# Kernel tuning notes

Measured on AMD Instinct MI355X. Metric: run time of the kernel, lower is better.

## Reference

```python
import jax, jax.numpy as jnp
import numpy as np

LATENT, COND, NEURONS, NHID = 64, 96, 128, 3
EPS = 1e-5


def setup_inputs() -> dict:
    key = jax.random.key(0)
    ks = jax.random.split(key, 20)
    B, N = 1024, 512
    z0 = jax.random.normal(ks[0], (B, LATENT), jnp.float32)
    # monotone time grid in [0,1]
    t = jnp.cumsum(jax.random.uniform(ks[1], (B, N, 1), jnp.float32), axis=1)
    t = t / t[:, -1:, :]
    condition = jax.random.normal(ks[2], (B, N, COND), jnp.float32)
    dims = [LATENT + COND] + [NEURONS] * NHID
    inp = {"z0": z0, "t": t, "condition": condition}
    for i in range(NHID):
        din, dout = dims[i], dims[i + 1]
        inp[f"W{i}"] = jax.random.normal(ks[3 + 4 * i], (din, dout), jnp.float32) / np.sqrt(din)
        inp[f"b{i}"] = jnp.zeros((dout,), jnp.float32)
        inp[f"g{i}"] = jnp.ones((dout,), jnp.float32)
        inp[f"beta{i}"] = jnp.zeros((dout,), jnp.float32)
    inp["Wo"] = jax.random.normal(ks[16], (NEURONS, LATENT), jnp.float32) / np.sqrt(NEURONS)
    inp["bo"] = jnp.zeros((LATENT,), jnp.float32)
    return inp


def _layer_norm(x, g, b):
    mu = jnp.mean(x, axis=-1, keepdims=True)
    var = jnp.var(x, axis=-1, keepdims=True)
    return (x - mu) * jax.lax.rsqrt(var + EPS) * g + b


def reference(z0, t, condition,
              W0, b0, g0, beta0,
              W1, b1, g1, beta1,
              W2, b2, g2, beta2,
              Wo, bo):
    # dropout is inference-mode identity
    hidden = [(W0, b0, g0, beta0), (W1, b1, g1, beta1), (W2, b2, g2, beta2)]

    def mlp(x):
        h = x
        for (W, b, g, be) in hidden:
            h = jnp.tanh(_layer_norm(h @ W + b, g, be))
        return h @ Wo + bo

    # time-major sequences for scan: [N-1, B, ...]
    cond_seq = jnp.swapaxes(condition[:, :-1, :], 0, 1)
    dt_seq = jnp.swapaxes(t[:, 1:, 0] - t[:, :-1, 0], 0, 1)[..., None]

    def step(z, inp):
        cond_i, dt_i = inp
        dz = mlp(jnp.concatenate([z, cond_i], axis=-1))
        z_next = z + dt_i * dz
        return z_next, z_next

    _, zs = jax.lax.scan(step, z0, (cond_seq, dt_seq))  # [N-1, B, D]
    z_traj = jnp.concatenate([z0[None], zs], axis=0)  # [N, B, D]
    return jnp.swapaxes(z_traj, 0, 1)  # [B, N, D]
```

## Files before the change

kernel.cpp:

```cpp
#include <hip/hip_runtime.h>
#include <stdint.h>

#define NSEQ 512
#define XS 168
#define AS 136
#define PS 36
#define EPS 1e-5f

typedef short bfrag __attribute__((ext_vector_type(8)));
typedef float f4 __attribute__((ext_vector_type(4)));
#define MFMA16 __builtin_amdgcn_mfma_f32_16x16x32_bf16

__device__ __forceinline__ unsigned short f2bf(float f){
  uint32_t u = __float_as_uint(f);
  u += 0x7FFFu + ((u>>16)&1u);
  return (unsigned short)(u>>16);
}
__device__ __forceinline__ uint32_t pk2bf(float a, float b){
  uint32_t r;
  asm("v_cvt_pk_bf16_f32 %0, %1, %2" : "=v"(r) : "v"(a), "v"(b));
  return r;
}
__device__ __forceinline__ float tanh_fast(float v){
  float e = __builtin_amdgcn_exp2f(v * 2.8853900817779268f);
  float r = __builtin_amdgcn_rcpf(e + 1.f);
  return fmaf(-2.f, r, 1.f);
}
__device__ __forceinline__ void lds_barrier(){
  asm volatile("s_waitcnt lgkmcnt(0)" ::: "memory");
  __builtin_amdgcn_s_barrier();
  asm volatile("" ::: "memory");
}

__device__ __forceinline__ void stats_write(const float (&h0)[4], const float (&h1)[4],
                                            float* __restrict__ part,
                                            const int w, const int lg, const int lc){
  const float s = ((h0[0]+h0[1])+(h0[2]+h0[3])) + ((h1[0]+h1[1])+(h1[2]+h1[3]));
  const float q = (fmaf(h0[0],h0[0], h0[1]*h0[1]) + fmaf(h0[2],h0[2], h0[3]*h0[3]))
                + (fmaf(h1[0],h1[0], h1[1]*h1[1]) + fmaf(h1[2],h1[2], h1[3]*h1[3]));
  *(float2*)(part + lc*PS + (w*4+lg)*2) = make_float2(s, q);
}

__device__ __forceinline__ void ln_tanh_store(const float (&h0)[4], const float (&h1)[4],
    const float (&gd)[2][4], const float (&bed)[2][4],
    const float* __restrict__ part, unsigned short* __restrict__ actb,
    const int w, const int lg, const int lc){
  const float* pr = part + lc*PS;
  const f4 p0=*(const f4*)(pr),    p1=*(const f4*)(pr+4),  p2=*(const f4*)(pr+8),  p3=*(const f4*)(pr+12);
  const f4 p4=*(const f4*)(pr+16), p5=*(const f4*)(pr+20), p6=*(const f4*)(pr+24), p7=*(const f4*)(pr+28);
  const float ss = (((p0.x+p0.z)+(p1.x+p1.z)) + ((p2.x+p2.z)+(p3.x+p3.z)))
                 + (((p4.x+p4.z)+(p5.x+p5.z)) + ((p6.x+p6.z)+(p7.x+p7.z)));
  const float qq = (((p0.y+p0.w)+(p1.y+p1.w)) + ((p2.y+p2.w)+(p3.y+p3.w)))
                 + (((p4.y+p4.w)+(p5.y+p5.w)) + ((p6.y+p6.w)+(p7.y+p7.w)));
  const float mu = ss * 0.0078125f;
  const float rs = rsqrtf(fmaf(qq, 0.0078125f, -mu*mu) + EPS);
  float e0[4], e1[4];
#pragma unroll
  for (int g=0; g<4; ++g){
    e0[g] = tanh_fast(fmaf((h0[g]-mu)*rs, gd[0][g], bed[0][g]));
    e1[g] = tanh_fast(fmaf((h1[g]-mu)*rs, gd[1][g], bed[1][g]));
  }
  uint4 pk4;
  pk4.x = pk2bf(e0[0],e0[1]); pk4.y = pk2bf(e0[2],e0[3]);
  pk4.z = pk2bf(e1[0],e1[1]); pk4.w = pk2bf(e1[2],e1[3]);
  *(uint4*)(actb + lc*AS + w*32 + lg*8) = pk4;
}

__global__ __launch_bounds__(256, 1)
void latent_ode_v9(const float* __restrict__ z0, const float* __restrict__ tt,
                   const float* __restrict__ cond,
                   const float* __restrict__ W0, const float* __restrict__ b0,
                   const float* __restrict__ g0, const float* __restrict__ be0,
                   const float* __restrict__ W1, const float* __restrict__ b1,
                   const float* __restrict__ g1, const float* __restrict__ be1,
                   const float* __restrict__ W2, const float* __restrict__ b2,
                   const float* __restrict__ g2, const float* __restrict__ be2,
                   const float* __restrict__ Wo, const float* __restrict__ bo,
                   float* __restrict__ out)
{
  __shared__ __align__(16) unsigned short xin[16*XS];
  __shared__ __align__(16) unsigned short act[16*AS];
  __shared__ __align__(16) float part[16*PS];

  const int t  = threadIdx.x;
  const int w  = t >> 6;
  const int l  = t & 63;
  const int lg = l >> 4;
  const int lc = l & 15;
  const int r0 = blockIdx.x * 16;
  const int zcol = w*16 + lg*4;

  bfrag A0z[2][2], A0c[2][3], A1f[2][4], A2f[2][4], Aof[4];
#pragma unroll
  for (int nt=0; nt<2; ++nt){
    const int col = w*32 + nt*4 + ((lc>>2)<<3) + (lc&3);
#pragma unroll
    for (int kt=0; kt<2; ++kt){
      union { bfrag v; unsigned short u[8]; } r;
#pragma unroll
      for (int j=0; j<8; ++j) r.u[j] = f2bf(W0[(size_t)(kt*32 + lg*8 + j)*128 + col]);
      A0z[nt][kt] = r.v;
    }
#pragma unroll
    for (int s=0; s<3; ++s){
      union { bfrag v; unsigned short u[8]; } r;
#pragma unroll
      for (int j=0; j<8; ++j) r.u[j] = f2bf(W0[(size_t)(64 + s*32 + lg*8 + j)*128 + col]);
      A0c[nt][s] = r.v;
    }
#pragma unroll
    for (int kt=0; kt<4; ++kt){
      union { bfrag v; unsigned short u[8]; } r1, r2;
#pragma unroll
      for (int j=0; j<8; ++j){
        const int k = kt*32 + lg*8 + j;
        r1.u[j] = f2bf(W1[(size_t)k*128 + col]);
        r2.u[j] = f2bf(W2[(size_t)k*128 + col]);
      }
      A1f[nt][kt] = r1.v; A2f[nt][kt] = r2.v;
    }
  }
#pragma unroll
  for (int kt=0; kt<4; ++kt){
    union { bfrag v; unsigned short u[8]; } r;
#pragma unroll
    for (int j=0; j<8; ++j)
      r.u[j] = f2bf(Wo[(size_t)(kt*32 + lg*8 + j)*64 + (w*16 + lc)]);
    Aof[kt] = r.v;
  }
  float bd0[2][4], gd0[2][4], bed0[2][4];
  float bd1[2][4], gd1[2][4], bed1[2][4];
  float bd2[2][4], gd2[2][4], bed2[2][4];
  float bo_d[4];
#pragma unroll
  for (int nt=0; nt<2; ++nt){
#pragma unroll
    for (int g=0; g<4; ++g){
      const int n = w*32 + lg*8 + nt*4 + g;
      bd0[nt][g]=b0[n]; gd0[nt][g]=g0[n]; bed0[nt][g]=be0[n];
      bd1[nt][g]=b1[n]; gd1[nt][g]=g1[n]; bed1[nt][g]=be1[n];
      bd2[nt][g]=b2[n]; gd2[nt][g]=g2[n]; bed2[nt][g]=be2[n];
    }
  }
#pragma unroll
  for (int g=0; g<4; ++g) bo_d[g] = bo[zcol + g];

  const float* tp = tt + (size_t)(r0+lc)*NSEQ;
  float tcv = tp[0], tnv = tp[1];

  f4 zr;
  {
    const f4 zv = *(const f4*)(z0 + (size_t)(r0+lc)*64 + zcol);
    zr = zv;
    *(f4*)(out + ((size_t)(r0+lc)*NSEQ)*64 + zcol) = zv;
    *(uint2*)(xin + lc*XS + zcol) = make_uint2(pk2bf(zv[0],zv[1]), pk2bf(zv[2],zv[3]));
  }

  const bool stgW = (t < 192);
  const int srow = t / 12, s8 = t - srow*12;
  const float* cptr = cond + ((size_t)(r0+srow)*NSEQ)*96 + s8*8;
  float4 pf0 = {0,0,0,0}, pf1 = {0,0,0,0};
  if (stgW){
    const float4 c0 = *(const float4*)(cptr);
    const float4 c1 = *(const float4*)(cptr + 4);
    uint4 u;
    u.x = pk2bf(c0.x,c0.y); u.y = pk2bf(c0.z,c0.w);
    u.z = pk2bf(c1.x,c1.y); u.w = pk2bf(c1.z,c1.w);
    *(uint4*)(xin + srow*XS + 64 + s8*8) = u;
    pf0 = *(const float4*)(cptr + 96);
    pf1 = *(const float4*)(cptr + 100);
  }
  lds_barrier();

  f4 apC[2];
  {
    const int o = lc*XS + 64 + lg*8;
    const bfrag c0 = *(const bfrag*)(xin + o);
    const bfrag c1 = *(const bfrag*)(xin + o + 32);
    const bfrag c2 = *(const bfrag*)(xin + o + 64);
    const f4 z4 = {0,0,0,0};
#pragma unroll
    for (int nt=0; nt<2; ++nt){
      f4 a = MFMA16(A0c[nt][0], c0, z4, 0,0,0);
      a = MFMA16(A0c[nt][1], c1, a, 0,0,0);
      a = MFMA16(A0c[nt][2], c2, a, 0,0,0);
      apC[nt] = a;
    }
  }
  lds_barrier();

  float h0[4], h1[4];
  for (int i=0; i<NSEQ-1; ++i){
    const int ip2 = (i+2 <= NSEQ-1) ? (i+2) : (NSEQ-1);
    const float tfv = tp[ip2];
    {
      const int o = lc*XS + lg*8;
      const bfrag bz0 = *(const bfrag*)(xin + o);
      const bfrag bz1 = *(const bfrag*)(xin + o + 32);
      const f4 z4 = {0,0,0,0};
      f4 c0 = MFMA16(A0z[0][0], bz0, z4, 0,0,0);
      f4 c1 = MFMA16(A0z[1][0], bz0, z4, 0,0,0);
      c0 = MFMA16(A0z[0][1], bz1, c0, 0,0,0);
      c1 = MFMA16(A0z[1][1], bz1, c1, 0,0,0);
#pragma unroll
      for (int g=0; g<4; ++g){
        h0[g] = (c0[g] + apC[0][g]) + bd0[0][g];
        h1[g] = (c1[g] + apC[1][g]) + bd0[1][g];
      }
      stats_write(h0, h1, part, w, lg, lc);
    }
    if (stgW){
      uint4 u;
      u.x = pk2bf(pf0.x,pf0.y); u.y = pk2bf(pf0.z,pf0.w);
      u.z = pk2bf(pf1.x,pf1.y); u.w = pk2bf(pf1.z,pf1.w);
      *(uint4*)(xin + srow*XS + 64 + s8*8) = u;
      if (i < NSEQ-2){
        pf0 = *(const float4*)(cptr + (size_t)(i+2)*96);
        pf1 = *(const float4*)(cptr + (size_t)(i+2)*96 + 4);
      }
    }
    lds_barrier();

    {
      const int o = lc*XS + 64 + lg*8;
      const bfrag c0 = *(const bfrag*)(xin + o);
      const bfrag c1 = *(const bfrag*)(xin + o + 32);
      const bfrag c2 = *(const bfrag*)(xin + o + 64);
      const f4 z4 = {0,0,0,0};
      f4 a0 = MFMA16(A0c[0][0], c0, z4, 0,0,0);
      f4 a1 = MFMA16(A0c[1][0], c0, z4, 0,0,0);
      a0 = MFMA16(A0c[0][1], c1, a0, 0,0,0);
      a1 = MFMA16(A0c[1][1], c1, a1, 0,0,0);
      a0 = MFMA16(A0c[0][2], c2, a0, 0,0,0);
      a1 = MFMA16(A0c[1][2], c2, a1, 0,0,0);
      ln_tanh_store(h0, h1, gd0, bed0, part, act, w, lg, lc);
      apC[0] = a0; apC[1] = a1;
    }
    lds_barrier();

    {
      const int o = lc*AS + lg*8;
      const bfrag b0f = *(const bfrag*)(act + o);
      const bfrag b1f = *(const bfrag*)(act + o + 32);
      const bfrag b2f = *(const bfrag*)(act + o + 64);
      const bfrag b3f = *(const bfrag*)(act + o + 96);
      const f4 z4 = {0,0,0,0};
      f4 ca0 = MFMA16(A1f[0][0], b0f, z4, 0,0,0);
      f4 cb0 = MFMA16(A1f[0][1], b1f, z4, 0,0,0);
      f4 ca1 = MFMA16(A1f[1][0], b0f, z4, 0,0,0);
      f4 cb1 = MFMA16(A1f[1][1], b1f, z4, 0,0,0);
      ca0 = MFMA16(A1f[0][2], b2f, ca0, 0,0,0);
      cb0 = MFMA16(A1f[0][3], b3f, cb0, 0,0,0);
      ca1 = MFMA16(A1f[1][2], b2f, ca1, 0,0,0);
      cb1 = MFMA16(A1f[1][3], b3f, cb1, 0,0,0);
#pragma unroll
      for (int g=0; g<4; ++g){
        h0[g] = (ca0[g]+cb0[g]) + bd1[0][g];
        h1[g] = (ca1[g]+cb1[g]) + bd1[1][g];
      }
      stats_write(h0, h1, part, w, lg, lc);
    }
    lds_barrier();

    ln_tanh_store(h0, h1, gd1, bed1, part, act, w, lg, lc);
    lds_barrier();

    {
      const int o = lc*AS + lg*8;
      const bfrag b0f = *(const bfrag*)(act + o);
      const bfrag b1f = *(const bfrag*)(act + o + 32);
      const bfrag b2f = *(const bfrag*)(act + o + 64);
      const bfrag b3f = *(const bfrag*)(act + o + 96);
      const f4 z4 = {0,0,0,0};
      f4 ca0 = MFMA16(A2f[0][0], b0f, z4, 0,0,0);
      f4 cb0 = MFMA16(A2f[0][1], b1f, z4, 0,0,0);
      f4 ca1 = MFMA16(A2f[1][0], b0f, z4, 0,0,0);
      f4 cb1 = MFMA16(A2f[1][1], b1f, z4, 0,0,0);
      ca0 = MFMA16(A2f[0][2], b2f, ca0, 0,0,0);
      cb0 = MFMA16(A2f[0][3], b3f, cb0, 0,0,0);
      ca1 = MFMA16(A2f[1][2], b2f, ca1, 0,0,0);
      cb1 = MFMA16(A2f[1][3], b3f, cb1, 0,0,0);
#pragma unroll
      for (int g=0; g<4; ++g){
        h0[g] = (ca0[g]+cb0[g]) + bd2[0][g];
        h1[g] = (ca1[g]+cb1[g]) + bd2[1][g];
      }
      stats_write(h0, h1, part, w, lg, lc);
    }
    lds_barrier();

    ln_tanh_store(h0, h1, gd2, bed2, part, act, w, lg, lc);
    lds_barrier();

    {
      const int o = lc*AS + lg*8;
      const bfrag b0f = *(const bfrag*)(act + o);
      const bfrag b1f = *(const bfrag*)(act + o + 32);
      const bfrag b2f = *(const bfrag*)(act + o + 64);
      const bfrag b3f = *(const bfrag*)(act + o + 96);
      const f4 z4 = {0,0,0,0};
      f4 aa = MFMA16(Aof[0], b0f, z4, 0,0,0);
      f4 ab = MFMA16(Aof[1], b1f, z4, 0,0,0);
      aa = MFMA16(Aof[2], b2f, aa, 0,0,0);
      ab = MFMA16(Aof[3], b3f, ab, 0,0,0);
      const float dt = tnv - tcv;
      f4 zn;
#pragma unroll
      for (int g=0; g<4; ++g) zn[g] = fmaf(dt, (aa[g]+ab[g]) + bo_d[g], zr[g]);
      zr = zn;
      *(f4*)(out + ((size_t)(r0+lc)*NSEQ + (size_t)(i+1))*64 + zcol) = zn;
      *(uint2*)(xin + lc*XS + zcol) = make_uint2(pk2bf(zn[0],zn[1]), pk2bf(zn[2],zn[3]));
      tcv = tnv; tnv = tfv;
    }
    lds_barrier();
  }
}

extern "C" void kernel_launch(void* const* d_in, const int* in_sizes, int n_in,
                              void* d_out, int out_size, void* d_ws, size_t ws_size,
                              hipStream_t stream) {
  const float* z0   = (const float*)d_in[0];
  const float* tt   = (const float*)d_in[1];
  const float* cond = (const float*)d_in[2];
  const float* W0   = (const float*)d_in[3];
  const float* b0   = (const float*)d_in[4];
  const float* g0   = (const float*)d_in[5];
  const float* be0  = (const float*)d_in[6];
  const float* W1   = (const float*)d_in[7];
  const float* b1   = (const float*)d_in[8];
  const float* g1   = (const float*)d_in[9];
  const float* be1  = (const float*)d_in[10];
  const float* W2   = (const float*)d_in[11];
  const float* b2   = (const float*)d_in[12];
  const float* g2   = (const float*)d_in[13];
  const float* be2  = (const float*)d_in[14];
  const float* Wo   = (const float*)d_in[15];
  const float* bo   = (const float*)d_in[16];
  float* out = (float*)d_out;

  hipLaunchKernelGGL(latent_ode_v9, dim3(64), dim3(256), 0, stream,
                     z0, tt, cond, W0, b0, g0, be0, W1, b1, g1, be1,
                     W2, b2, g2, be2, Wo, bo, out);
}
```

Before: 1.111 ms.

## Fuse LayerNorm+tanh into consumer GEMM to halve per-step barriers

```diff
diff --git a/kernel.cpp b/kernel.cpp
--- a/kernel.cpp
+++ b/kernel.cpp
@@ -2,9 +2,10 @@
 #include <stdint.h>
 
 #define NSEQ 512
-#define XS 168
-#define AS 136
+#define XS 104
+#define HS 132
 #define PS 36
+#define ZS 76
 #define EPS 1e-5f
 
 typedef short bfrag __attribute__((ext_vector_type(8)));
@@ -41,10 +42,8 @@
   *(float2*)(part + lc*PS + (w*4+lg)*2) = make_float2(s, q);
 }
 
-__device__ __forceinline__ void ln_tanh_store(const float (&h0)[4], const float (&h1)[4],
-    const float (&gd)[2][4], const float (&bed)[2][4],
-    const float* __restrict__ part, unsigned short* __restrict__ actb,
-    const int w, const int lg, const int lc){
+__device__ __forceinline__ void ln_mu_rs(const float* __restrict__ part, const int lc,
+                                         float& mu, float& rs){
   const float* pr = part + lc*PS;
   const f4 p0=*(const f4*)(pr),    p1=*(const f4*)(pr+4),  p2=*(const f4*)(pr+8),  p3=*(const f4*)(pr+12);
   const f4 p4=*(const f4*)(pr+16), p5=*(const f4*)(pr+20), p6=*(const f4*)(pr+24), p7=*(const f4*)(pr+28);
@@ -52,35 +51,55 @@
                  + (((p4.x+p4.z)+(p5.x+p5.z)) + ((p6.x+p6.z)+(p7.x+p7.z)));
   const float qq = (((p0.y+p0.w)+(p1.y+p1.w)) + ((p2.y+p2.w)+(p3.y+p3.w)))
                  + (((p4.y+p4.w)+(p5.y+p5.w)) + ((p6.y+p6.w)+(p7.y+p7.w)));
-  const float mu = ss * 0.0078125f;
-  const float rs = rsqrtf(fmaf(qq, 0.0078125f, -mu*mu) + EPS);
-  float e0[4], e1[4];
-#pragma unroll
-  for (int g=0; g<4; ++g){
-    e0[g] = tanh_fast(fmaf((h0[g]-mu)*rs, gd[0][g], bed[0][g]));
-    e1[g] = tanh_fast(fmaf((h1[g]-mu)*rs, gd[1][g], bed[1][g]));
-  }
-  uint4 pk4;
-  pk4.x = pk2bf(e0[0],e0[1]); pk4.y = pk2bf(e0[2],e0[3]);
-  pk4.z = pk2bf(e1[0],e1[1]); pk4.w = pk2bf(e1[2],e1[3]);
-  *(uint4*)(actb + lc*AS + w*32 + lg*8) = pk4;
+  mu = ss * 0.0078125f;
+  rs = rsqrtf(fmaf(qq, 0.0078125f, -mu*mu) + EPS);
+}
+
+__device__ __forceinline__ void consume_ln(const float* __restrict__ hb,
+    const float* __restrict__ part, const uint32_t* __restrict__ pg,
+    bfrag (&B)[4], const int lg, const int lc){
+  float mu, rs;
+  ln_mu_rs(part, lc, mu, rs);
+#pragma unroll
+  for (int kt=0; kt<4; ++kt){
+    const float* hp = hb + lc*HS + kt*32 + lg*8;
+    const f4 ha = *(const f4*)(hp);
+    const f4 hc = *(const f4*)(hp + 4);
+    const uint4 q0 = *(const uint4*)(pg + kt*32 + lg*8);
+    const uint4 q1 = *(const uint4*)(pg + kt*32 + lg*8 + 4);
+    const uint32_t gu[8] = {q0.x,q0.y,q0.z,q0.w,q1.x,q1.y,q1.z,q1.w};
+    float e[8];
+#pragma unroll
+    for (int j=0;j<8;++j){
+      const float h = (j<4)? ha[j] : hc[j-4];
+      const float gg = __uint_as_float(gu[j] & 0xFFFF0000u);
+      const float bb = __uint_as_float(gu[j] << 16);
+      e[j] = tanh_fast(fmaf((h - mu)*rs, gg, bb));
+    }
+    union { bfrag v; uint32_t u[4]; } r;
+    r.u[0]=pk2bf(e[0],e[1]); r.u[1]=pk2bf(e[2],e[3]);
+    r.u[2]=pk2bf(e[4],e[5]); r.u[3]=pk2bf(e[6],e[7]);
+    B[kt]=r.v;
+  }
 }
 
 __global__ __launch_bounds__(256, 1)
-void latent_ode_v9(const float* __restrict__ z0, const float* __restrict__ tt,
-                   const float* __restrict__ cond,
-                   const float* __restrict__ W0, const float* __restrict__ b0,
-                   const float* __restrict__ g0, const float* __restrict__ be0,
-                   const float* __restrict__ W1, const float* __restrict__ b1,
-                   const float* __restrict__ g1, const float* __restrict__ be1,
-                   const float* __restrict__ W2, const float* __restrict__ b2,
-                   const float* __restrict__ g2, const float* __restrict__ be2,
-                   const float* __restrict__ Wo, const float* __restrict__ bo,
-                   float* __restrict__ out)
+void latent_ode_v15(const float* __restrict__ z0, const float* __restrict__ tt,
+                    const float* __restrict__ cond,
+                    const float* __restrict__ W0, const float* __restrict__ b0,
+                    const float* __restrict__ g0, const float* __restrict__ be0,
+                    const float* __restrict__ W1, const float* __restrict__ b1,
+                    const float* __restrict__ g1, const float* __restrict__ be1,
+                    const float* __restrict__ W2, const float* __restrict__ b2,
+                    const float* __restrict__ g2, const float* __restrict__ be2,
+                    const float* __restrict__ Wo, const float* __restrict__ bo,
+                    float* __restrict__ out)
 {
   __shared__ __align__(16) unsigned short xin[16*XS];
-  __shared__ __align__(16) unsigned short act[16*AS];
-  __shared__ __align__(16) float part[16*PS];
+  __shared__ __align__(16) unsigned short zbuf[16*ZS];
+  __shared__ __align__(16) float hA[16*HS], hB[16*HS];
+  __shared__ __align__(16) float partA[16*PS], partB[16*PS];
+  __shared__ __align__(16) uint32_t pgb[3*128];
 
   const int t  = threadIdx.x;
   const int w  = t >> 6;
@@ -128,22 +147,26 @@
       r.u[j] = f2bf(Wo[(size_t)(kt*32 + lg*8 + j)*64 + (w*16 + lc)]);
     Aof[kt] = r.v;
   }
-  float bd0[2][4], gd0[2][4], bed0[2][4];
-  float bd1[2][4], gd1[2][4], bed1[2][4];
-  float bd2[2][4], gd2[2][4], bed2[2][4];
-  float bo_d[4];
+  float bd0[2][4], bd1[2][4], bd2[2][4], bo_d[4];
 #pragma unroll
   for (int nt=0; nt<2; ++nt){
 #pragma unroll
     for (int g=0; g<4; ++g){
       const int n = w*32 + lg*8 + nt*4 + g;
-      bd0[nt][g]=b0[n]; gd0[nt][g]=g0[n]; bed0[nt][g]=be0[n];
-      bd1[nt][g]=b1[n]; gd1[nt][g]=g1[n]; bed1[nt][g]=be1[n];
-      bd2[nt][g]=b2[n]; gd2[nt][g]=g2[n]; bed2[nt][g]=be2[n];
+      bd0[nt][g]=b0[n]; bd1[nt][g]=b1[n]; bd2[nt][g]=b2[n];
     }
   }
 #pragma unroll
   for (int g=0; g<4; ++g) bo_d[g] = bo[zcol + g];
+
+  for (int idx=t; idx<384; idx+=256){
+    const int n = idx & 127;
+    float gv, bv;
+    if (idx < 128){ gv = g0[n]; bv = be0[n]; }
+    else if (idx < 256){ gv = g1[n]; bv = be1[n]; }
+    else { gv = g2[n]; bv = be2[n]; }
+    pgb[idx] = pk2bf(bv, gv);
+  }
 
   const float* tp = tt + (size_t)(r0+lc)*NSEQ;
   float tcv = tp[0], tnv = tp[1];
@@ -152,8 +175,8 @@
   {
     const f4 zv = *(const f4*)(z0 + (size_t)(r0+lc)*64 + zcol);
     zr = zv;
+    *(uint2*)(zbuf + lc*ZS + zcol) = make_uint2(pk2bf(zv[0],zv[1]), pk2bf(zv[2],zv[3]));
     *(f4*)(out + ((size_t)(r0+lc)*NSEQ)*64 + zcol) = zv;
-    *(uint2*)(xin + lc*XS + zcol) = make_uint2(pk2bf(zv[0],zv[1]), pk2bf(zv[2],zv[3]));
   }
 
   const bool stgW = (t < 192);
@@ -166,7 +189,7 @@
     uint4 u;
     u.x = pk2bf(c0.x,c0.y); u.y = pk2bf(c0.z,c0.w);
     u.z = pk2bf(c1.x,c1.y); u.w = pk2bf(c1.z,c1.w);
-    *(uint4*)(xin + srow*XS + 64 + s8*8) = u;
+    *(uint4*)(xin + srow*XS + s8*8) = u;
     pf0 = *(const float4*)(cptr + 96);
     pf1 = *(const float4*)(cptr + 100);
   }
@@ -174,7 +197,7 @@
 
   f4 apC[2];
   {
-    const int o = lc*XS + 64 + lg*8;
+    const int o = lc*XS + lg*8;
     const bfrag c0 = *(const bfrag*)(xin + o);
     const bfrag c1 = *(const bfrag*)(xin + o + 32);
     const bfrag c2 = *(const bfrag*)(xin + o + 64);
@@ -194,26 +217,31 @@
     const int ip2 = (i+2 <= NSEQ-1) ? (i+2) : (NSEQ-1);
     const float tfv = tp[ip2];
     {
-      const int o = lc*XS + lg*8;
-      const bfrag bz0 = *(const bfrag*)(xin + o);
-      const bfrag bz1 = *(const bfrag*)(xin + o + 32);
+      const int o = lc*ZS + lg*8;
+      const bfrag bz0 = *(const bfrag*)(zbuf + o);
+      const bfrag bz1 = *(const bfrag*)(zbuf + o + 32);
       const f4 z4 = {0,0,0,0};
       f4 c0 = MFMA16(A0z[0][0], bz0, z4, 0,0,0);
       f4 c1 = MFMA16(A0z[1][0], bz0, z4, 0,0,0);
       c0 = MFMA16(A0z[0][1], bz1, c0, 0,0,0);
       c1 = MFMA16(A0z[1][1], bz1, c1, 0,0,0);
+      f4 vh0, vh1;
 #pragma unroll
       for (int g=0; g<4; ++g){
         h0[g] = (c0[g] + apC[0][g]) + bd0[0][g];
         h1[g] = (c1[g] + apC[1][g]) + bd0[1][g];
-      }
-      stats_write(h0, h1, part, w, lg, lc);
+        vh0[g] = h0[g]; vh1[g] = h1[g];
+      }
+      stats_write(h0, h1, partA, w, lg, lc);
+      float* hw = hA + lc*HS + w*32 + lg*8;
+      *(f4*)(hw) = vh0;
+      *(f4*)(hw + 4) = vh1;
     }
     if (stgW){
       uint4 u;
       u.x = pk2bf(pf0.x,pf0.y); u.y = pk2bf(pf0.z,pf0.w);
       u.z = pk2bf(pf1.x,pf1.y); u.w = pk2bf(pf1.z,pf1.w);
-      *(uint4*)(xin + srow*XS + 64 + s8*8) = u;
+      *(uint4*)(xin + srow*XS + s8*8) = u;
       if (i < NSEQ-2){
         pf0 = *(const float4*)(cptr + (size_t)(i+2)*96);
         pf1 = *(const float4*)(cptr + (size_t)(i+2)*96 + 4);
@@ -222,7 +250,7 @@
     lds_barrier();
 
     {
-      const int o = lc*XS + 64 + lg*8;
+      const int o = lc*XS + lg*8;
       const bfrag c0 = *(const bfrag*)(xin + o);
       const bfrag c1 = *(const bfrag*)(xin + o + 32);
       const bfrag c2 = *(const bfrag*)(xin + o + 64);
@@ -233,83 +261,73 @@
       a1 = MFMA16(A0c[1][1], c1, a1, 0,0,0);
       a0 = MFMA16(A0c[0][2], c2, a0, 0,0,0);
       a1 = MFMA16(A0c[1][2], c2, a1, 0,0,0);
-      ln_tanh_store(h0, h1, gd0, bed0, part, act, w, lg, lc);
-      apC[0] = a0; apC[1] = a1;
-    }
-    lds_barrier();
-
-    {
-      const int o = lc*AS + lg*8;
-      const bfrag b0f = *(const bfrag*)(act + o);
-      const bfrag b1f = *(const bfrag*)(act + o + 32);
-      const bfrag b2f = *(const bfrag*)(act + o + 64);
-      const bfrag b3f = *(const bfrag*)(act + o + 96);
-      const f4 z4 = {0,0,0,0};
-      f4 ca0 = MFMA16(A1f[0][0], b0f, z4, 0,0,0);
-      f4 cb0 = MFMA16(A1f[0][1], b1f, z4, 0,0,0);
-      f4 ca1 = MFMA16(A1f[1][0], b0f, z4, 0,0,0);
-      f4 cb1 = MFMA16(A1f[1][1], b1f, z4, 0,0,0);
-      ca0 = MFMA16(A1f[0][2], b2f, ca0, 0,0,0);
-      cb0 = MFMA16(A1f[0][3], b3f, cb0, 0,0,0);
-      ca1 = MFMA16(A1f[1][2], b2f, ca1, 0,0,0);
-      cb1 = MFMA16(A1f[1][3], b3f, cb1, 0,0,0);
+
+      bfrag B[4];
+      consume_ln(hA, partA, pgb, B, lg, lc);
+      f4 ca0 = MFMA16(A1f[0][0], B[0], z4, 0,0,0);
+      f4 cb0 = MFMA16(A1f[0][1], B[1], z4, 0,0,0);
+      f4 ca1 = MFMA16(A1f[1][0], B[0], z4, 0,0,0);
+      f4 cb1 = MFMA16(A1f[1][1], B[1], z4, 0,0,0);
+      ca0 = MFMA16(A1f[0][2], B[2], ca0, 0,0,0);
+      cb0 = MFMA16(A1f[0][3], B[3], cb0, 0,0,0);
+      ca1 = MFMA16(A1f[1][2], B[2], ca1, 0,0,0);
+      cb1 = MFMA16(A1f[1][3], B[3], cb1, 0,0,0);
+      f4 vh0, vh1;
 #pragma unroll
       for (int g=0; g<4; ++g){
         h0[g] = (ca0[g]+cb0[g]) + bd1[0][g];
         h1[g] = (ca1[g]+cb1[g]) + bd1[1][g];
-      }
-      stats_write(h0, h1, part, w, lg, lc);
+        vh0[g] = h0[g]; vh1[g] = h1[g];
+      }
+      stats_write(h0, h1, partB, w, lg, lc);
+      float* hw = hB + lc*HS + w*32 + lg*8;
+      *(f4*)(hw) = vh0;
+      *(f4*)(hw + 4) = vh1;
+      apC[0] = a0; apC[1] = a1;
     }
     lds_barrier();
 
-    ln_tanh_store(h0, h1, gd1, bed1, part, act, w, lg, lc);
-    lds_barrier();
-
     {
-      const int o = lc*AS + lg*8;
-      const bfrag b0f = *(const bfrag*)(act + o);
-      const bfrag b1f = *(const bfrag*)(act + o + 32);
-      const bfrag b2f = *(const bfrag*)(act + o + 64);
-      const bfrag b3f = *(const bfrag*)(act + o + 96);
       const f4 z4 = {0,0,0,0};
-      f4 ca0 = MFMA16(A2f[0][0], b0f, z4, 0,0,0);
-      f4 cb0 = MFMA16(A2f[0][1], b1f, z4, 0,0,0);
-      f4 ca1 = MFMA16(A2f[1][0], b0f, z4, 0,0,0);
-      f4 cb1 = MFMA16(A2f[1][1], b1f, z4, 0,0,0);
-      ca0 = MFMA16(A2f[0][2], b2f, ca0, 0,0,0);
-      cb0 = MFMA16(A2f[0][3], b3f, cb0, 0,0,0);
-      ca1 = MFMA16(A2f[1][2], b2f, ca1, 0,0,0);
-      cb1 = MFMA16(A2f[1][3], b3f, cb1, 0,0,0);
+      bfrag B[4];
+      consume_ln(hB, partB, pgb + 128, B, lg, lc);
+      f4 ca0 = MFMA16(A2f[0][0], B[0], z4, 0,0,0);
+      f4 cb0 = MFMA16(A2f[0][1], B[1], z4, 0,0,0);
+      f4 ca1 = MFMA16(A2f[1][0], B[0], z4, 0,0,0);
+      f4 cb1 = MFMA16(A2f[1][1], B[1], z4, 0,0,0);
+      ca0 = MFMA16(A2f[0][2], B[2], ca0, 0,0,0);
+      cb0 = MFMA16(A2f[0][3], B[3], cb0, 0,0,0);
+      ca1 = MFMA16(A2f[1][2], B[2], ca1, 0,0,0);
+      cb1 = MFMA16(A2f[1][3], B[3], cb1, 0,0,0);
+      f4 vh0, vh1;
 #pragma unroll
       for (int g=0; g<4; ++g){
         h0[g] = (ca0[g]+cb0[g]) + bd2[0][g];
         h1[g] = (ca1[g]+cb1[g]) + bd2[1][g];
-      }
-      stats_write(h0, h1, part, w, lg, lc);
+        vh0[g] = h0[g]; vh1[g] = h1[g];
+      }
+      stats_write(h0, h1, partA, w, lg, lc);
+      float* hw = hA + lc*HS + w*32 + lg*8;
+      *(f4*)(hw) = vh0;
+      *(f4*)(hw + 4) = vh1;
     }
     lds_barrier();
 
-    ln_tanh_store(h0, h1, gd2, bed2, part, act, w, lg, lc);
-    lds_barrier();
-
     {
-      const int o = lc*AS + lg*8;
-      const bfrag b0f = *(const bfrag*)(act + o);
-      const bfrag b1f = *(const bfrag*)(act + o + 32);
-      const bfrag b2f = *(const bfrag*)(act + o + 64);
-      const bfrag b3f = *(const bfrag*)(act + o + 96);
       const f4 z4 = {0,0,0,0};
-      f4 aa = MFMA16(Aof[0], b0f, z4, 0,0,0);
-      f4 ab = MFMA16(Aof[1], b1f, z4, 0,0,0);
-      aa = MFMA16(Aof[2], b2f, aa, 0,0,0);
-      ab = MFMA16(Aof[3], b3f, ab, 0,0,0);
+      bfrag B[4];
+      consume_ln(hA, partA, pgb + 256, B, lg, lc);
+      f4 aa = MFMA16(Aof[0], B[0], z4, 0,0,0);
+      f4 ab = MFMA16(Aof[1], B[1], z4, 0,0,0);
+      aa = MFMA16(Aof[2], B[2], aa, 0,0,0);
+      ab = MFMA16(Aof[3], B[3], ab, 0,0,0);
       const float dt = tnv - tcv;
       f4 zn;
 #pragma unroll
       for (int g=0; g<4; ++g) zn[g] = fmaf(dt, (aa[g]+ab[g]) + bo_d[g], zr[g]);
       zr = zn;
+      *(uint2*)(zbuf + lc*ZS + zcol) = make_uint2(pk2bf(zn[0],zn[1]), pk2bf(zn[2],zn[3]));
       *(f4*)(out + ((size_t)(r0+lc)*NSEQ + (size_t)(i+1))*64 + zcol) = zn;
-      *(uint2*)(xin + lc*XS + zcol) = make_uint2(pk2bf(zn[0],zn[1]), pk2bf(zn[2],zn[3]));
       tcv = tnv; tnv = tfv;
     }
     lds_barrier();
@@ -338,7 +356,7 @@
   const float* bo   = (const float*)d_in[16];
   float* out = (float*)d_out;
 
-  hipLaunchKernelGGL(latent_ode_v9, dim3(64), dim3(256), 0, stream,
+  hipLaunchKernelGGL(latent_ode_v15, dim3(64), dim3(256), 0, stream,
                      z0, tt, cond, W0, b0, g0, be0, W1, b1, g1, be1,
                      W2, b2, g2, be2, Wo, bo, out);
 }
```

After: 2.017 ms. 1.82x slower.
